# Kernel tuning notes

Measured on AMD Instinct MI355X. Metric: run time of the kernel, lower is better.

## Reference

```python
import jax, jax.numpy as jnp
import numpy as np

M_SIGMA = 1.0 * 0.997 / 3.0  # args.m * 0.997 / 3


def setup_inputs() -> dict:
    key = jax.random.key(0)
    k1, k2 = jax.random.split(key)
    B, D = 64, 512        # batch (sketches+shapes), embedding dim
    P = 256               # points per cloud
    embeddings = jax.random.normal(k1, (B, D), dtype=jnp.float32)
    xyz = jax.random.normal(k2, (B, P, 3), dtype=jnp.float32)
    return {"embeddings": embeddings, "xyz": xyz}


def _chamfer_all_pairs(shapes):
    # shapes: [M, P, 3]. Returns cd[i, j] = chamfer(shapes[i], shapes[j]),
    # chamfer = mean_p min_q ||x_p - y_q||^2 + mean_q min_p ||x_p - y_q||^2
    sq = jnp.sum(shapes * shapes, axis=-1)                  # [M, P]
    inner = jnp.einsum('ipd,jqd->ijpq', shapes, shapes)     # [M, M, P, P]
    d2 = sq[:, None, :, None] + sq[None, :, None, :] - 2.0 * inner
    cd = jnp.min(d2, axis=3).mean(axis=2) + jnp.min(d2, axis=2).mean(axis=2)
    return cd  # [M, M]


def reference(embeddings, xyz):
    # L2-normalize embeddings along feature dim
    emb = embeddings / jnp.linalg.norm(embeddings, axis=1, keepdims=True)
    B = emb.shape[0]
    mb = B // 2
    shapes = xyz[mb:]                                       # [mb, P, 3]
    sketch_feat, shape_feat = emb[:mb], emb[mb:]            # [mb, D] each
    inner_dot = sketch_feat @ shape_feat.T                  # [mb, mb]
    cd = _chamfer_all_pairs(shapes)                         # [mb, mb]
    real_dist = (cd ** 2) / (2.0 * M_SIGMA ** 2)
    p = jax.nn.softmax(-real_dist, axis=1)
    p_hat = jax.nn.softmax(inner_dot, axis=1)               # use_softmax=True
    reg = jnp.mean(jnp.abs(p_hat - p))                      # use_KL=False
    return reg
```

## Files before the change

### kernel.cpp

```cpp
#include <hip/hip_runtime.h>
#include <math.h>


typedef float f32x2 __attribute__((ext_vector_type(2)));

__device__ __forceinline__ float waveReduceSum64(float v) {
    #pragma unroll
    for (int m = 32; m > 0; m >>= 1) v += __shfl_xor(v, m, 64);
    return v;
}

__global__ __launch_bounds__(256) void pairs_kernel(const float* __restrict__ emb,
                                                    const float* __restrict__ xyz,
                                                    float* __restrict__ cdHalf,
                                                    float* __restrict__ dots) {
    const int t = threadIdx.x;
    const int b = blockIdx.x;

    __shared__ __align__(16) float S[3 * 256];
    __shared__ float red[4];
    float* Sx = S;
    float* Sy = S + 256;
    float* Sz = S + 512;

    if (b < 992) {
        const int pb  = b >> 1;
        const int dir = b & 1;
        int i = 0, rem = pb;
        while (rem >= (31 - i)) { rem -= (31 - i); ++i; }
        const int j = i + 1 + rem;

        const int outer = dir ? j : i;
        const int inner = dir ? i : j;

        const float* Po = xyz + (32 + outer) * 768;
        const float* Pi = xyz + (32 + inner) * 768;

        const float ix = Pi[3*t], iy = Pi[3*t+1], iz = Pi[3*t+2];
        Sx[t] = ix; Sy[t] = iy; Sz[t] = iz;
        const float px = Po[3*t], py = Po[3*t+1], pz = Po[3*t+2];
        __syncthreads();

        const f32x2 Px = {px, px}, Py = {py, py}, Pz = {pz, pz};
        f32x2 m0 = {3.4e38f, 3.4e38f}, m1 = {3.4e38f, 3.4e38f};

        #pragma unroll 4
        for (int s = 0; s < 256; s += 4) {
            const float4 vx = *(const float4*)&Sx[s];
            const float4 vy = *(const float4*)&Sy[s];
            const float4 vz = *(const float4*)&Sz[s];
            {
                const f32x2 bx = {vx.x, vx.y}, by = {vy.x, vy.y}, bz = {vz.x, vz.y};
                f32x2 dx = Px - bx, dy = Py - by, dz = Pz - bz;
                f32x2 d = dx*dx + dy*dy + dz*dz;
                m0.x = fminf(m0.x, d.x); m0.y = fminf(m0.y, d.y);
            }
            {
                const f32x2 bx = {vx.z, vx.w}, by = {vy.z, vy.w}, bz = {vz.z, vz.w};
                f32x2 dx = Px - bx, dy = Py - by, dz = Pz - bz;
                f32x2 d = dx*dx + dy*dy + dz*dz;
                m1.x = fminf(m1.x, d.x); m1.y = fminf(m1.y, d.y);
            }
        }
        const float mn = fminf(fminf(m0.x, m0.y), fminf(m1.x, m1.y));

        float v = waveReduceSum64(mn);
        if ((t & 63) == 0) red[t >> 6] = v;
        __syncthreads();
        if (t == 0)
            cdHalf[b] = (red[0] + red[1] + red[2] + red[3]) * (1.0f / 256.0f);
    } else {
        const int i = b - 992;
        float* rowi = S;
        const float* Ei = emb + i * 512;
        rowi[t]       = Ei[t];
        rowi[t + 256] = Ei[t + 256];
        __syncthreads();

        const int w    = t >> 6;
        const int lane = t & 63;

        float ni = 0.0f;
        #pragma unroll
        for (int m = 0; m < 8; ++m) { float a = rowi[lane + 64*m]; ni += a*a; }
        ni = waveReduceSum64(ni);

        for (int j = w; j < 32; j += 4) {
            const float* Ej = emb + (32 + j) * 512;
            float dot = 0.0f, nj = 0.0f;
            #pragma unroll
            for (int m = 0; m < 8; ++m) {
                float a  = rowi[lane + 64*m];
                float bv = Ej[lane + 64*m];
                dot += a * bv;
                nj  += bv * bv;
            }
            dot = waveReduceSum64(dot);
            nj  = waveReduceSum64(nj);
            if (lane == 0) dots[i * 32 + j] = dot * rsqrtf(ni * nj);
        }
    }
}

__global__ __launch_bounds__(1024) void finish_kernel(const float* __restrict__ cdHalf,
                                                      const float* __restrict__ dots,
                                                      float* __restrict__ out) {
    const int t = threadIdx.x;
    const int i = t >> 5;
    const int j = t & 31;
    const float inv_denom = 1.0f / (2.0f * (0.997f / 3.0f) * (0.997f / 3.0f));

    float c;
    if (i == j) {
        c = 0.0f;
    } else {
        const int a  = min(i, j), bb = max(i, j);
        const int pb = a * 31 - (a * (a - 1)) / 2 + (bb - a - 1);
        c = cdHalf[2 * pb] + cdHalf[2 * pb + 1];
    }
    float s = -(c * c) * inv_denom;
    float h = dots[t];

    float m1 = s;
    #pragma unroll
    for (int k = 16; k > 0; k >>= 1) m1 = fmaxf(m1, __shfl_xor(m1, k, 32));
    float e1 = expf(s - m1);
    float sum1 = e1;
    #pragma unroll
    for (int k = 16; k > 0; k >>= 1) sum1 += __shfl_xor(sum1, k, 32);
    float p = e1 / sum1;

    float m2 = h;
    #pragma unroll
    for (int k = 16; k > 0; k >>= 1) m2 = fmaxf(m2, __shfl_xor(m2, k, 32));
    float e2 = expf(h - m2);
    float sum2 = e2;
    #pragma unroll
    for (int k = 16; k > 0; k >>= 1) sum2 += __shfl_xor(sum2, k, 32);
    float ph = e2 / sum2;

    float a = fabsf(ph - p);
    a = waveReduceSum64(a);

    __shared__ float red[16];
    if ((t & 63) == 0) red[t >> 6] = a;
    __syncthreads();
    if (t == 0) {
        float tot = 0.0f;
        #pragma unroll
        for (int k = 0; k < 16; ++k) tot += red[k];
        out[0] = tot * (1.0f / 1024.0f);
    }
}

extern "C" void kernel_launch(void* const* d_in, const int* in_sizes, int n_in,
                              void* d_out, int out_size, void* d_ws, size_t ws_size,
                              hipStream_t stream) {
    const float* emb = (const float*)d_in[0];
    const float* xyz = (const float*)d_in[1];
    float* cdHalf = (float*)d_ws;
    float* dots   = cdHalf + 1024;
    float* out    = (float*)d_out;

    hipLaunchKernelGGL(pairs_kernel, dim3(1024), dim3(256), 0, stream, emb, xyz, cdHalf, dots);
    hipLaunchKernelGGL(finish_kernel, dim3(1), dim3(1024), 0, stream, cdHalf, dots, out);
}
```

Measured before the change: 66.55 us.

## Fuse finish into pairs kernel via last-block ticket and expand distance algebra

Merges the two launches into one kernel. Each block publishes its partial results to device globals, and the last block to take a ticket from an atomic counter computes both softmaxes and the final mean. The inner chamfer loop now uses the expanded form |q|^2 - 2p·q, with -2q and |q|^2 precomputed in shared memory, so each pair costs three FMAs instead of subtract-square-add. This removes a second kernel launch and its dependency gap, in exchange for an atomic counter, memory fences, and some numeric change from the expanded distance.

```diff
diff --git a/kernel.cpp b/kernel.cpp
--- a/kernel.cpp
+++ b/kernel.cpp
@@ -3,6 +3,10 @@
 
 
 typedef float f32x2 __attribute__((ext_vector_type(2)));
+
+__device__ float g_cdHalf[992];
+__device__ float g_dots[1024];
+__device__ unsigned int g_counter = 0;
 
 __device__ __forceinline__ float waveReduceSum64(float v) {
     #pragma unroll
@@ -10,35 +14,35 @@
     return v;
 }
 
-__global__ __launch_bounds__(256) void pairs_kernel(const float* __restrict__ emb,
-                                                    const float* __restrict__ xyz,
-                                                    float* __restrict__ cdHalf,
-                                                    float* __restrict__ dots) {
+__global__ __launch_bounds__(256, 4) void fused_kernel(const float* __restrict__ emb,
+                                                       const float* __restrict__ xyz,
+                                                       float* __restrict__ out) {
     const int t = threadIdx.x;
     const int b = blockIdx.x;
 
-    __shared__ __align__(16) float S[3 * 256];
+    __shared__ __align__(16) float S[4 * 256];
     __shared__ float red[4];
-    float* Sx = S;
-    float* Sy = S + 256;
-    float* Sz = S + 512;
+    __shared__ unsigned int ticket;
 
     if (b < 992) {
         const int pb  = b >> 1;
         const int dir = b & 1;
-        int i = 0, rem = pb;
-        while (rem >= (31 - i)) { rem -= (31 - i); ++i; }
-        const int j = i + 1 + rem;
-
-        const int outer = dir ? j : i;
-        const int inner = dir ? i : j;
+        int ii = 0, rem = pb;
+        while (rem >= (31 - ii)) { rem -= (31 - ii); ++ii; }
+        const int jj = ii + 1 + rem;
+        const int outer = dir ? jj : ii;
+        const int inner = dir ? ii : jj;
 
         const float* Po = xyz + (32 + outer) * 768;
         const float* Pi = xyz + (32 + inner) * 768;
 
-        const float ix = Pi[3*t], iy = Pi[3*t+1], iz = Pi[3*t+2];
-        Sx[t] = ix; Sy[t] = iy; Sz[t] = iz;
+        const float qx = Pi[3*t], qy = Pi[3*t+1], qz = Pi[3*t+2];
+        S[t]       = -2.0f * qx;
+        S[t + 256] = -2.0f * qy;
+        S[t + 512] = -2.0f * qz;
+        S[t + 768] = qx*qx + qy*qy + qz*qz;
         const float px = Po[3*t], py = Po[3*t+1], pz = Po[3*t+2];
+        const float pp = px*px + py*py + pz*pz;
         __syncthreads();
 
         const f32x2 Px = {px, px}, Py = {py, py}, Pz = {pz, pz};
@@ -46,29 +50,34 @@
 
         #pragma unroll 4
         for (int s = 0; s < 256; s += 4) {
-            const float4 vx = *(const float4*)&Sx[s];
-            const float4 vy = *(const float4*)&Sy[s];
-            const float4 vz = *(const float4*)&Sz[s];
+            const float4 vx = *(const float4*)&S[s];
+            const float4 vy = *(const float4*)&S[s + 256];
+            const float4 vz = *(const float4*)&S[s + 512];
+            const float4 vw = *(const float4*)&S[s + 768];
             {
-                const f32x2 bx = {vx.x, vx.y}, by = {vy.x, vy.y}, bz = {vz.x, vz.y};
-                f32x2 dx = Px - bx, dy = Py - by, dz = Pz - bz;
-                f32x2 d = dx*dx + dy*dy + dz*dz;
-                m0.x = fminf(m0.x, d.x); m0.y = fminf(m0.y, d.y);
+                f32x2 e = {vw.x, vw.y};
+                e = Pz * (f32x2){vz.x, vz.y} + e;
+                e = Py * (f32x2){vy.x, vy.y} + e;
+                e = Px * (f32x2){vx.x, vx.y} + e;
+                m0.x = fminf(m0.x, e.x); m0.y = fminf(m0.y, e.y);
             }
             {
-                const f32x2 bx = {vx.z, vx.w}, by = {vy.z, vy.w}, bz = {vz.z, vz.w};
-                f32x2 dx = Px - bx, dy = Py - by, dz = Pz - bz;
-                f32x2 d = dx*dx + dy*dy + dz*dz;
-                m1.x = fminf(m1.x, d.x); m1.y = fminf(m1.y, d.y);
+                f32x2 e = {vw.z, vw.w};
+                e = Pz * (f32x2){vz.z, vz.w} + e;
+                e = Py * (f32x2){vy.z, vy.w} + e;
+                e = Px * (f32x2){vx.z, vx.w} + e;
+                m1.x = fminf(m1.x, e.x); m1.y = fminf(m1.y, e.y);
             }
         }
-        const float mn = fminf(fminf(m0.x, m0.y), fminf(m1.x, m1.y));
+        const float mn = fminf(fminf(m0.x, m0.y), fminf(m1.x, m1.y)) + pp;
 
         float v = waveReduceSum64(mn);
         if ((t & 63) == 0) red[t >> 6] = v;
         __syncthreads();
-        if (t == 0)
-            cdHalf[b] = (red[0] + red[1] + red[2] + red[3]) * (1.0f / 256.0f);
+        if (t == 0) {
+            const float val = (red[0] + red[1] + red[2] + red[3]) * (1.0f / 256.0f);
+            __hip_atomic_store(&g_cdHalf[b], val, __ATOMIC_RELAXED, __HIP_MEMORY_SCOPE_AGENT);
+        }
     } else {
         const int i = b - 992;
         float* rowi = S;
@@ -97,71 +106,78 @@
             }
             dot = waveReduceSum64(dot);
             nj  = waveReduceSum64(nj);
-            if (lane == 0) dots[i * 32 + j] = dot * rsqrtf(ni * nj);
+            if (lane == 0)
+                __hip_atomic_store(&g_dots[i * 32 + j], dot * rsqrtf(ni * nj),
+                                   __ATOMIC_RELAXED, __HIP_MEMORY_SCOPE_AGENT);
         }
     }
-}
 
-__global__ __launch_bounds__(1024) void finish_kernel(const float* __restrict__ cdHalf,
-                                                      const float* __restrict__ dots,
-                                                      float* __restrict__ out) {
-    const int t = threadIdx.x;
-    const int i = t >> 5;
-    const int j = t & 31;
+    __threadfence();
+    __syncthreads();
+    if (t == 0)
+        ticket = __hip_atomic_fetch_add(&g_counter, 1u, __ATOMIC_ACQ_REL,
+                                        __HIP_MEMORY_SCOPE_AGENT) & 1023u;
+    __syncthreads();
+    if (ticket != 1023u) return;
+    __threadfence();
+
+    const int fi = t >> 3;
+    const int jb = (t & 7) << 2;
     const float inv_denom = 1.0f / (2.0f * (0.997f / 3.0f) * (0.997f / 3.0f));
 
-    float c;
-    if (i == j) {
-        c = 0.0f;
-    } else {
-        const int a  = min(i, j), bb = max(i, j);
-        const int pb = a * 31 - (a * (a - 1)) / 2 + (bb - a - 1);
-        c = cdHalf[2 * pb] + cdHalf[2 * pb + 1];
+    float sv[4], hv[4];
+    #pragma unroll
+    for (int k = 0; k < 4; ++k) {
+        const int j = jb + k;
+        float c = 0.0f;
+        if (fi != j) {
+            const int a  = fi < j ? fi : j;
+            const int bb = fi < j ? j : fi;
+            const int pq = a * 31 - (a * (a - 1)) / 2 + (bb - a - 1);
+            const float c0 = __hip_atomic_load(&g_cdHalf[2*pq],     __ATOMIC_RELAXED, __HIP_MEMORY_SCOPE_AGENT);
+            const float c1 = __hip_atomic_load(&g_cdHalf[2*pq + 1], __ATOMIC_RELAXED, __HIP_MEMORY_SCOPE_AGENT);
+            c = c0 + c1;
+        }
+        sv[k] = -(c * c) * inv_denom;
+        hv[k] = __hip_atomic_load(&g_dots[fi * 32 + jb + k], __ATOMIC_RELAXED, __HIP_MEMORY_SCOPE_AGENT);
     }
-    float s = -(c * c) * inv_denom;
-    float h = dots[t];
 
-    float m1 = s;
+    float mx1 = fmaxf(fmaxf(sv[0], sv[1]), fmaxf(sv[2], sv[3]));
+    float mx2 = fmaxf(fmaxf(hv[0], hv[1]), fmaxf(hv[2], hv[3]));
     #pragma unroll
-    for (int k = 16; k > 0; k >>= 1) m1 = fmaxf(m1, __shfl_xor(m1, k, 32));
-    float e1 = expf(s - m1);
-    float sum1 = e1;
+    for (int m = 1; m <= 4; m <<= 1) {
+        mx1 = fmaxf(mx1, __shfl_xor(mx1, m, 64));
+        mx2 = fmaxf(mx2, __shfl_xor(mx2, m, 64));
+    }
+    float e1[4], e2[4], sum1 = 0.0f, sum2 = 0.0f;
     #pragma unroll
-    for (int k = 16; k > 0; k >>= 1) sum1 += __shfl_xor(sum1, k, 32);
-    float p = e1 / sum1;
+    for (int k = 0; k < 4; ++k) {
+        e1[k] = expf(sv[k] - mx1); sum1 += e1[k];
+        e2[k] = expf(hv[k] - mx2); sum2 += e2[k];
+    }
+    #pragma unroll
+    for (int m = 1; m <= 4; m <<= 1) {
+        sum1 += __shfl_xor(sum1, m, 64);
+        sum2 += __shfl_xor(sum2, m, 64);
+    }
+    float acc = 0.0f;
+    #pragma unroll
+    for (int k = 0; k < 4; ++k) acc += fabsf(e2[k] / sum2 - e1[k] / sum1);
 
-    float m2 = h;
-    #pragma unroll
-    for (int k = 16; k > 0; k >>= 1) m2 = fmaxf(m2, __shfl_xor(m2, k, 32));
-    float e2 = expf(h - m2);
-    float sum2 = e2;
-    #pragma unroll
-    for (int k = 16; k > 0; k >>= 1) sum2 += __shfl_xor(sum2, k, 32);
-    float ph = e2 / sum2;
-
-    float a = fabsf(ph - p);
-    a = waveReduceSum64(a);
-
-    __shared__ float red[16];
-    if ((t & 63) == 0) red[t >> 6] = a;
+    acc = waveReduceSum64(acc);
+    if ((t & 63) == 0) red[t >> 6] = acc;
     __syncthreads();
-    if (t == 0) {
-        float tot = 0.0f;
-        #pragma unroll
-        for (int k = 0; k < 16; ++k) tot += red[k];
-        out[0] = tot * (1.0f / 1024.0f);
-    }
+    if (t == 0)
+        out[0] = (red[0] + red[1] + red[2] + red[3]) * (1.0f / 1024.0f);
 }
 
 extern "C" void kernel_launch(void* const* d_in, const int* in_sizes, int n_in,
                               void* d_out, int out_size, void* d_ws, size_t ws_size,
                               hipStream_t stream) {
+    (void)in_sizes; (void)n_in; (void)out_size; (void)d_ws; (void)ws_size;
     const float* emb = (const float*)d_in[0];
     const float* xyz = (const float*)d_in[1];
-    float* cdHalf = (float*)d_ws;
-    float* dots   = cdHalf + 1024;
-    float* out    = (float*)d_out;
+    float* out = (float*)d_out;
 
-    hipLaunchKernelGGL(pairs_kernel, dim3(1024), dim3(256), 0, stream, emb, xyz, cdHalf, dots);
-    hipLaunchKernelGGL(finish_kernel, dim3(1), dim3(1024), 0, stream, cdHalf, dots, out);
+    hipLaunchKernelGGL(fused_kernel, dim3(1024), dim3(256), 0, stream, emb, xyz, out);
 }
```

Result: slower. 136.1 us (+104.6%).

## Map one chamfer direction per wavefront with expanded-distance FMAs and scalar loads

Applied to the files above, without the earlier changes.

Each wavefront now handles one directed shape pair, with each lane holding four outer points in registers. The inner cloud is read through uniform (scalar) global loads instead of being staged in LDS. The squared distance is rewritten as |q|^2 - 2p·q with a three-FMA chain, and |p|^2 is added after the min, so block-level syncs and the LDS reduction go away. This cuts the block count from 1024 to 280, which lowers parallelism per CU, and the expanded form can lose some floating-point precision through cancellation.

```diff
diff --git a/kernel.cpp b/kernel.cpp
--- a/kernel.cpp
+++ b/kernel.cpp
@@ -17,60 +17,59 @@
     const int t = threadIdx.x;
     const int b = blockIdx.x;
 
-    __shared__ __align__(16) float S[3 * 256];
-    __shared__ float red[4];
-    float* Sx = S;
-    float* Sy = S + 256;
-    float* Sz = S + 512;
+    __shared__ float S[512];
 
-    if (b < 992) {
-        const int pb  = b >> 1;
-        const int dir = b & 1;
-        int i = 0, rem = pb;
-        while (rem >= (31 - i)) { rem -= (31 - i); ++i; }
-        const int j = i + 1 + rem;
-
-        const int outer = dir ? j : i;
-        const int inner = dir ? i : j;
+    if (b < 248) {
+        const int w    = t >> 6;
+        const int lane = t & 63;
+        const int pairIdx = __builtin_amdgcn_readfirstlane((b << 2) | w);
+        const int pb  = pairIdx >> 1;
+        const int dir = pairIdx & 1;
+        int ii = 0, rem = pb;
+        while (rem >= (31 - ii)) { rem -= (31 - ii); ++ii; }
+        const int jj = ii + 1 + rem;
+        const int outer = dir ? jj : ii;
+        const int inner = dir ? ii : jj;
 
         const float* Po = xyz + (32 + outer) * 768;
-        const float* Pi = xyz + (32 + inner) * 768;
+        const float* Qf = xyz + (32 + inner) * 768;
 
-        const float ix = Pi[3*t], iy = Pi[3*t+1], iz = Pi[3*t+2];
-        Sx[t] = ix; Sy[t] = iy; Sz[t] = iz;
-        const float px = Po[3*t], py = Po[3*t+1], pz = Po[3*t+2];
-        __syncthreads();
+        float px[4], py[4], pz[4], pp[4];
+        #pragma unroll
+        for (int k = 0; k < 4; ++k) {
+            const float* P = Po + 3 * (lane + 64 * k);
+            px[k] = P[0]; py[k] = P[1]; pz[k] = P[2];
+            pp[k] = px[k] * px[k] + py[k] * py[k] + pz[k] * pz[k];
+        }
+        const f32x2 X01 = {-2.f * px[0], -2.f * px[1]}, X23 = {-2.f * px[2], -2.f * px[3]};
+        const f32x2 Y01 = {-2.f * py[0], -2.f * py[1]}, Y23 = {-2.f * py[2], -2.f * py[3]};
+        const f32x2 Z01 = {-2.f * pz[0], -2.f * pz[1]}, Z23 = {-2.f * pz[2], -2.f * pz[3]};
 
-        const f32x2 Px = {px, px}, Py = {py, py}, Pz = {pz, pz};
-        f32x2 m0 = {3.4e38f, 3.4e38f}, m1 = {3.4e38f, 3.4e38f};
+        f32x2 m01 = {3.4e38f, 3.4e38f}, m23 = {3.4e38f, 3.4e38f};
 
-        #pragma unroll 4
-        for (int s = 0; s < 256; s += 4) {
-            const float4 vx = *(const float4*)&Sx[s];
-            const float4 vy = *(const float4*)&Sy[s];
-            const float4 vz = *(const float4*)&Sz[s];
-            {
-                const f32x2 bx = {vx.x, vx.y}, by = {vy.x, vy.y}, bz = {vz.x, vz.y};
-                f32x2 dx = Px - bx, dy = Py - by, dz = Pz - bz;
-                f32x2 d = dx*dx + dy*dy + dz*dz;
-                m0.x = fminf(m0.x, d.x); m0.y = fminf(m0.y, d.y);
-            }
-            {
-                const f32x2 bx = {vx.z, vx.w}, by = {vy.z, vy.w}, bz = {vz.z, vz.w};
-                f32x2 dx = Px - bx, dy = Py - by, dz = Pz - bz;
-                f32x2 d = dx*dx + dy*dy + dz*dz;
-                m1.x = fminf(m1.x, d.x); m1.y = fminf(m1.y, d.y);
-            }
+        #pragma unroll 8
+        for (int s = 0; s < 256; ++s) {
+            const float qx = Qf[3 * s];
+            const float qy = Qf[3 * s + 1];
+            const float qz = Qf[3 * s + 2];
+            const float qw = qx * qx + qy * qy + qz * qz;
+            const f32x2 QX = {qx, qx}, QY = {qy, qy}, QZ = {qz, qz}, QW = {qw, qw};
+            f32x2 e01 = Z01 * QZ + QW;
+            e01 = Y01 * QY + e01;
+            e01 = X01 * QX + e01;
+            f32x2 e23 = Z23 * QZ + QW;
+            e23 = Y23 * QY + e23;
+            e23 = X23 * QX + e23;
+            m01.x = fminf(m01.x, e01.x); m01.y = fminf(m01.y, e01.y);
+            m23.x = fminf(m23.x, e23.x); m23.y = fminf(m23.y, e23.y);
         }
-        const float mn = fminf(fminf(m0.x, m0.y), fminf(m1.x, m1.y));
 
-        float v = waveReduceSum64(mn);
-        if ((t & 63) == 0) red[t >> 6] = v;
-        __syncthreads();
-        if (t == 0)
-            cdHalf[b] = (red[0] + red[1] + red[2] + red[3]) * (1.0f / 256.0f);
+        float ssum = (m01.x + pp[0]) + (m01.y + pp[1]) +
+                     (m23.x + pp[2]) + (m23.y + pp[3]);
+        ssum = waveReduceSum64(ssum);
+        if (lane == 0) cdHalf[pairIdx] = ssum * (1.0f / 256.0f);
     } else {
-        const int i = b - 992;
+        const int i = b - 248;
         float* rowi = S;
         const float* Ei = emb + i * 512;
         rowi[t]       = Ei[t];
@@ -82,7 +81,7 @@
 
         float ni = 0.0f;
         #pragma unroll
-        for (int m = 0; m < 8; ++m) { float a = rowi[lane + 64*m]; ni += a*a; }
+        for (int m = 0; m < 8; ++m) { float a = rowi[lane + 64 * m]; ni += a * a; }
         ni = waveReduceSum64(ni);
 
         for (int j = w; j < 32; j += 4) {
@@ -90,8 +89,8 @@
             float dot = 0.0f, nj = 0.0f;
             #pragma unroll
             for (int m = 0; m < 8; ++m) {
-                float a  = rowi[lane + 64*m];
-                float bv = Ej[lane + 64*m];
+                float a  = rowi[lane + 64 * m];
+                float bv = Ej[lane + 64 * m];
                 dot += a * bv;
                 nj  += bv * bv;
             }
@@ -156,12 +155,13 @@
 extern "C" void kernel_launch(void* const* d_in, const int* in_sizes, int n_in,
                               void* d_out, int out_size, void* d_ws, size_t ws_size,
                               hipStream_t stream) {
+    (void)in_sizes; (void)n_in; (void)out_size; (void)ws_size;
     const float* emb = (const float*)d_in[0];
     const float* xyz = (const float*)d_in[1];
     float* cdHalf = (float*)d_ws;
     float* dots   = cdHalf + 1024;
     float* out    = (float*)d_out;
 
-    hipLaunchKernelGGL(pairs_kernel, dim3(1024), dim3(256), 0, stream, emb, xyz, cdHalf, dots);
+    hipLaunchKernelGGL(pairs_kernel, dim3(280), dim3(256), 0, stream, emb, xyz, cdHalf, dots);
     hipLaunchKernelGGL(finish_kernel, dim3(1), dim3(1024), 0, stream, cdHalf, dots, out);
 }
```

Result: no change. 67.19 us (+1.0%).
